# Kernel tuning notes

Hardware: AMD Instinct MI355X
Metric: run time of the kernel (lower is better)

## Reference

```python
import jax, jax.numpy as jnp
import numpy as np

# Module constants (from init_kwargs / defaults)
CIN, COUT = 128, 64
H, W = 256, 256
X0, X1 = -50.0, 50.0
Y0, Y1 = -50.0, 50.0
Z0, Z1 = -3.0, 5.0
XRES = (X1 - X0) / W
YRES = (Y1 - Y0) / H
EPS = 1e-5


def setup_inputs() -> dict:
    key = jax.random.key(0)
    ks = jax.random.split(key, 24)
    B, N = 4, 100000
    # Points: x,y in [-55,55], z in [-3.5,5.5] so some points fall outside range (tests valid mask)
    xy = jax.random.uniform(ks[0], (B, N, 2), minval=-55.0, maxval=55.0)
    z = jax.random.uniform(ks[1], (B, N, 1), minval=-3.5, maxval=5.5)
    points = jnp.concatenate([xy, z], axis=-1).astype(jnp.float32)
    features = jax.random.normal(ks[2], (B, N, CIN), dtype=jnp.float32)

    def lin(k, fan_in, shape):
        return jax.random.uniform(k, shape, minval=-1.0, maxval=1.0) / np.sqrt(fan_in)

    inp = dict(points=points, features=features)
    # point_mlp: Linear(131,64) -> BN1d(64) -> ReLU -> Linear(64,64)
    inp['w1'] = lin(ks[3], CIN + 3, (CIN + 3, COUT)).astype(jnp.float32)
    inp['b1'] = lin(ks[4], CIN + 3, (COUT,)).astype(jnp.float32)
    inp['bn1_g'] = jax.random.uniform(ks[5], (COUT,), minval=0.5, maxval=1.5)
    inp['bn1_b'] = 0.1 * jax.random.normal(ks[6], (COUT,))
    inp['bn1_m'] = 0.1 * jax.random.normal(ks[7], (COUT,))
    inp['bn1_v'] = jax.random.uniform(ks[8], (COUT,), minval=0.5, maxval=1.5)
    inp['w2'] = lin(ks[9], COUT, (COUT, COUT)).astype(jnp.float32)
    inp['b2'] = lin(ks[10], COUT, (COUT,)).astype(jnp.float32)
    # bev_conv: Conv(64,64,3)+BN2d+ReLU, Conv(64,64,3)+BN2d+ReLU  (OIHW kernels)
    fan = COUT * 9
    inp['cw1'] = lin(ks[11], fan, (COUT, COUT, 3, 3)).astype(jnp.float32)
    inp['cb1'] = lin(ks[12], fan, (COUT,)).astype(jnp.float32)
    inp['cbn1_g'] = jax.random.uniform(ks[13], (COUT,), minval=0.5, maxval=1.5)
    inp['cbn1_b'] = 0.1 * jax.random.normal(ks[14], (COUT,))
    inp['cbn1_m'] = 0.1 * jax.random.normal(ks[15], (COUT,))
    inp['cbn1_v'] = jax.random.uniform(ks[16], (COUT,), minval=0.5, maxval=1.5)
    inp['cw2'] = lin(ks[17], fan, (COUT, COUT, 3, 3)).astype(jnp.float32)
    inp['cb2'] = lin(ks[18], fan, (COUT,)).astype(jnp.float32)
    inp['cbn2_g'] = jax.random.uniform(ks[19], (COUT,), minval=0.5, maxval=1.5)
    inp['cbn2_b'] = 0.1 * jax.random.normal(ks[20], (COUT,))
    inp['cbn2_m'] = 0.1 * jax.random.normal(ks[21], (COUT,))
    inp['cbn2_v'] = jax.random.uniform(ks[22], (COUT,), minval=0.5, maxval=1.5)
    return {k: jnp.asarray(v, jnp.float32) for k, v in inp.items()}


def _bn(x, g, b, m, v, axis):
    shape = [1] * x.ndim
    shape[axis] = -1
    r = lambda a: a.reshape(shape)
    return (x - r(m)) * jax.lax.rsqrt(r(v) + EPS) * r(g) + r(b)


def _conv(x, w, b):
    y = jax.lax.conv_general_dilated(x, w, (1, 1), 'SAME',
                                     dimension_numbers=('NCHW', 'OIHW', 'NCHW'))
    return y + b[None, :, None, None]


def _forward(points, features, w1, b1, bn1_g, bn1_b, bn1_m, bn1_v, w2, b2,
             cw1, cb1, cbn1_g, cbn1_b, cbn1_m, cbn1_v,
             cw2, cb2, cbn2_g, cbn2_b, cbn2_m, cbn2_v):
    B, N, _ = features.shape
    x, y, z = points[..., 0], points[..., 1], points[..., 2]
    valid = ((x >= X0) & (x < X1) & (y >= Y0) & (y < Y1) & (z >= Z0) & (z < Z1))  # (B,N)
    col = jnp.clip(((x - X0) / XRES).astype(jnp.int32), 0, W - 1)
    row = jnp.clip(((y - Y0) / YRES).astype(jnp.int32), 0, H - 1)

    # position encoding (normalized coords)
    pos = jnp.stack([(x - X0) / (X1 - X0), (y - Y0) / (Y1 - Y0), (z - Z0) / (Z1 - Z0)], axis=-1)
    combined = jnp.concatenate([features, pos], axis=-1)  # (B,N,C+3)

    # point MLP (BN in inference mode with running stats)
    h = jnp.einsum('bnc,co->bno', combined, w1) + b1
    h = jax.nn.relu(_bn(h, bn1_g, bn1_b, bn1_m, bn1_v, axis=2))
    h = jnp.einsum('bnc,co->bno', h, w2) + b2  # (B,N,COUT)

    # scatter-max into BEV grid; bev initialized to zeros, so floor at 0
    seg = (jnp.arange(B, dtype=jnp.int32)[:, None] * H + row) * W + col  # (B,N)
    NEG = jnp.float32(-jnp.inf)
    vals = jnp.where(valid[..., None], h, NEG).reshape(B * N, COUT)
    m = jax.ops.segment_max(vals, seg.reshape(-1), num_segments=B * H * W)
    bev = jnp.maximum(m, 0.0).reshape(B, H, W, COUT).transpose(0, 3, 1, 2)  # (B,COUT,H,W)

    # BEV conv stack
    bev = jax.nn.relu(_bn(_conv(bev, cw1, cb1), cbn1_g, cbn1_b, cbn1_m, cbn1_v, axis=1))
    bev = jax.nn.relu(_bn(_conv(bev, cw2, cb2), cbn2_g, cbn2_b, cbn2_m, cbn2_v, axis=1))
    return bev


def reference(points, features, w1, b1, bn1_g, bn1_b, bn1_m, bn1_v, w2, b2,
              cw1, cb1, cbn1_g, cbn1_b, cbn1_m, cbn1_v,
              cw2, cb2, cbn2_g, cbn2_b, cbn2_m, cbn2_v):
    return _forward(points, features, w1, b1, bn1_g, bn1_b, bn1_m, bn1_v, w2, b2,
                    cw1, cb1, cbn1_g, cbn1_b, cbn1_m, cbn1_v,
                    cw2, cb2, cbn2_g, cbn2_b, cbn2_m, cbn2_v)
```

## Files before the change

kernel.cpp:

```cpp
#include <hip/hip_runtime.h>
#include <hip/hip_bf16.h>

typedef __attribute__((ext_vector_type(8))) short short8;
typedef __attribute__((ext_vector_type(4))) float floatx4;

static __device__ __forceinline__ unsigned short f2bf(float f) {
    unsigned int u = __float_as_uint(f);
    unsigned int r = (u + 0x7FFFu + ((u >> 16) & 1u)) >> 16;
    return (unsigned short)r;
}

static __device__ __forceinline__ short8 cvt8(const float* __restrict__ p) {
    const float4 f0 = *reinterpret_cast<const float4*>(p);
    const float4 f1 = *reinterpret_cast<const float4*>(p + 4);
    union { short8 s; __hip_bfloat162 h[4]; } u;
    u.h[0] = __float22bfloat162_rn(make_float2(f0.x, f0.y));
    u.h[1] = __float22bfloat162_rn(make_float2(f0.z, f0.w));
    u.h[2] = __float22bfloat162_rn(make_float2(f1.x, f1.y));
    u.h[3] = __float22bfloat162_rn(make_float2(f1.z, f1.w));
    return u.s;
}
static __device__ __forceinline__ uint4 cvt8u(const float* __restrict__ p) {
    const float4 f0 = *reinterpret_cast<const float4*>(p);
    const float4 f1 = *reinterpret_cast<const float4*>(p + 4);
    union { uint4 u; __hip_bfloat162 h[4]; } w;
    w.h[0] = __float22bfloat162_rn(make_float2(f0.x, f0.y));
    w.h[1] = __float22bfloat162_rn(make_float2(f0.z, f0.w));
    w.h[2] = __float22bfloat162_rn(make_float2(f1.x, f1.y));
    w.h[3] = __float22bfloat162_rn(make_float2(f1.z, f1.w));
    return w.u;
}

#define BATCH 4
#define NPTS 100000
#define CIN 128
#define COUT 64
#define HH 256
#define WW 256
#define HP 258
#define WP 258

#define OFF_BUF2 0
#define SZ_BUF   (BATCH * HP * WP * COUT * 2)
#define OFF_WB1  (OFF_BUF2 + SZ_BUF)
#define SZ_WB    (9 * COUT * COUT * 2)
#define OFF_WB2  (OFF_WB1 + SZ_WB)
#define OFF_BIAS1 (OFF_WB2 + SZ_WB)
#define OFF_BIAS2 (OFF_BIAS1 + 256)
#define OFF_W1T  (OFF_BIAS2 + 256)
#define OFF_W1POS (OFF_W1T + 64 * 128 * 2)
#define OFF_B1F  (OFF_W1POS + 768)
#define OFF_W2T  (OFF_B1F + 256)
#define OFF_B2F  (OFF_W2T + 64 * 64 * 2)

__global__ void prep_weights(const float* __restrict__ cw1, const float* __restrict__ cb1,
                             const float* __restrict__ g1, const float* __restrict__ bb1,
                             const float* __restrict__ m1, const float* __restrict__ v1,
                             const float* __restrict__ cw2, const float* __restrict__ cb2,
                             const float* __restrict__ g2, const float* __restrict__ bb2,
                             const float* __restrict__ m2, const float* __restrict__ v2,
                             unsigned short* __restrict__ Wb1, unsigned short* __restrict__ Wb2,
                             float* __restrict__ bias1, float* __restrict__ bias2) {
    int idx = blockIdx.x * 256 + threadIdx.x;
    int l = idx / 36864;
    int r = idx - l * 36864;
    int ci = r & 63;
    int co = (r >> 6) & 63;
    int tap = r >> 12;
    const float* w  = l ? cw2 : cw1;
    const float* g  = l ? g2  : g1;
    const float* v  = l ? v2  : v1;
    float s = g[co] * rsqrtf(v[co] + 1e-5f);
    float wv = w[(co * 64 + ci) * 9 + tap] * s;
    (l ? Wb2 : Wb1)[(tap * 64 + co) * 64 + ci] = f2bf(wv);
    if (tap == 0 && ci == 0) {
        const float* cb = l ? cb2 : cb1;
        const float* bb = l ? bb2 : bb1;
        const float* m  = l ? m2  : m1;
        (l ? bias2 : bias1)[co] = s * (cb[co] - m[co]) + bb[co];
    }
}

__global__ void prep_mlp(const float* __restrict__ w1, const float* __restrict__ b1,
                         const float* __restrict__ g, const float* __restrict__ bb,
                         const float* __restrict__ m, const float* __restrict__ v,
                         const float* __restrict__ w2, const float* __restrict__ b2,
                         unsigned short* __restrict__ w1T, float* __restrict__ w1pos,
                         float* __restrict__ b1f,
                         unsigned short* __restrict__ w2T, float* __restrict__ b2f) {
    int idx = blockIdx.x * 256 + threadIdx.x;
    if (idx < 8192) {
        int co = idx >> 7, k = idx & 127;
        float rs = g[co] * rsqrtf(v[co] + 1e-5f);
        w1T[idx] = f2bf(w1[k * 64 + co] * rs);
        if (k < 3) w1pos[k * 64 + co] = w1[(128 + k) * 64 + co] * rs;
        if (k == 0) b1f[co] = (b1[co] - m[co]) * rs + bb[co];
    }
    if (idx < 4096) {
        int co = idx >> 6, k = idx & 63;
        w2T[idx] = f2bf(w2[k * 64 + co]);
        if (k == 0) b2f[co] = b2[co];
    }
}

__global__ void ring_zero(unsigned short* __restrict__ buf2) {
    int idx = blockIdx.x * 256 + threadIdx.x;
    if (idx >= 4 * 1028 * 8) return;
    int c8 = idx & 7;
    int rest = idx >> 3;
    int p = rest % 1028;
    int b = rest / 1028;
    int x, y;
    if (p < 258)      { y = 0;   x = p; }
    else if (p < 516) { y = 257; x = p - 258; }
    else if (p < 772) { x = 0;   y = p - 516 + 1; }
    else              { x = 257; y = p - 772 + 1; }
    unsigned short* dst = buf2 + (((b * HP + y) * WP + x) * 64 + c8 * 8);
    uint4 z = {0u, 0u, 0u, 0u};
    *reinterpret_cast<uint4*>(dst) = z;
}

#define HSTR 72
#define VSTR 68
__global__ __launch_bounds__(256) void mlp_gemm_scatter(
        const float* __restrict__ points, const float* __restrict__ features,
        const unsigned short* __restrict__ w1T, const float* __restrict__ w1pos,
        const float* __restrict__ b1f,
        const unsigned short* __restrict__ w2T, const float* __restrict__ b2f,
        float* __restrict__ bev ) {
    __shared__ unsigned short ldsH[128 * HSTR];
    __shared__ unsigned short ldsV[128 * VSTR];
    __shared__ float4 ldsPos[128];

    const int tid = threadIdx.x;
    const int w = tid >> 6, lane = tid & 63, n = lane & 15, q = lane >> 4;
    const int m0 = w * 32;
    const long pt0 = (long)blockIdx.x * 128;

    if (lane < 32) {
        const long pt = pt0 + m0 + lane;
        const float x = points[pt * 3 + 0];
        const float y = points[pt * 3 + 1];
        const float z = points[pt * 3 + 2];
        const bool valid = (x >= -50.f) & (x < 50.f) & (y >= -50.f) & (y < 50.f) &
                           (z >= -3.f) & (z < 5.f);
        int cell = -1;
        if (valid) {
            int col = (int)((x + 50.f) / 0.390625f); col = min(max(col, 0), 255);
            int row = (int)((y + 50.f) / 0.390625f); row = min(max(row, 0), 255);
            int b = pt >= 300000 ? 3 : (pt >= 200000 ? 2 : (pt >= 100000 ? 1 : 0));
            cell = (b * HH + row) * WW + col;
        }
        float4 v;
        v.x = (x + 50.f) * 0.01f;
        v.y = (y + 50.f) * 0.01f;
        v.z = (z + 3.f) * 0.125f;
        v.w = __int_as_float(cell);
        ldsPos[m0 + lane] = v;
    }

    floatx4 acc[2][4];
    #pragma unroll
    for (int mt = 0; mt < 2; ++mt)
        #pragma unroll
        for (int nt = 0; nt < 4; ++nt) acc[mt][nt] = (floatx4){0.f, 0.f, 0.f, 0.f};

    #pragma unroll
    for (int ks = 0; ks < 4; ++ks) {
        short8 bf[4];
        #pragma unroll
        for (int nt = 0; nt < 4; ++nt)
            bf[nt] = *reinterpret_cast<const short8*>(w1T + (nt * 16 + n) * 128 + ks * 32 + q * 8);
        #pragma unroll
        for (int mt = 0; mt < 2; ++mt) {
            short8 a = cvt8(features + (pt0 + m0 + mt * 16 + n) * CIN + ks * 32 + q * 8);
            #pragma unroll
            for (int nt = 0; nt < 4; ++nt)
                acc[mt][nt] = __builtin_amdgcn_mfma_f32_16x16x32_bf16(a, bf[nt], acc[mt][nt], 0, 0, 0);
        }
    }

    float w1p[3][4], bs1[4];
    #pragma unroll
    for (int nt = 0; nt < 4; ++nt) {
        bs1[nt] = b1f[nt * 16 + n];
        #pragma unroll
        for (int j = 0; j < 3; ++j) w1p[j][nt] = w1pos[j * 64 + nt * 16 + n];
    }

    #pragma unroll
    for (int mt = 0; mt < 2; ++mt)
        #pragma unroll
        for (int r = 0; r < 4; ++r) {
            const int mm = m0 + mt * 16 + q * 4 + r;
            const float4 pos = ldsPos[mm];
            #pragma unroll
            for (int nt = 0; nt < 4; ++nt) {
                float hv = acc[mt][nt][r] + bs1[nt]
                         + pos.x * w1p[0][nt] + pos.y * w1p[1][nt] + pos.z * w1p[2][nt];
                ldsH[mm * HSTR + nt * 16 + n] = f2bf(fmaxf(hv, 0.f));
            }
        }

    floatx4 acc2[2][4];
    #pragma unroll
    for (int mt = 0; mt < 2; ++mt)
        #pragma unroll
        for (int nt = 0; nt < 4; ++nt) acc2[mt][nt] = (floatx4){0.f, 0.f, 0.f, 0.f};

    #pragma unroll
    for (int ks = 0; ks < 2; ++ks) {
        short8 bf[4];
        #pragma unroll
        for (int nt = 0; nt < 4; ++nt)
            bf[nt] = *reinterpret_cast<const short8*>(w2T + (nt * 16 + n) * 64 + ks * 32 + q * 8);
        #pragma unroll
        for (int mt = 0; mt < 2; ++mt) {
            short8 a = *reinterpret_cast<const short8*>(
                &ldsH[(m0 + mt * 16 + n) * HSTR + ks * 32 + q * 8]);
            #pragma unroll
            for (int nt = 0; nt < 4; ++nt)
                acc2[mt][nt] = __builtin_amdgcn_mfma_f32_16x16x32_bf16(a, bf[nt], acc2[mt][nt], 0, 0, 0);
        }
    }

    float bs2[4];
    #pragma unroll
    for (int nt = 0; nt < 4; ++nt) bs2[nt] = b2f[nt * 16 + n];

    #pragma unroll
    for (int mt = 0; mt < 2; ++mt)
        #pragma unroll
        for (int r = 0; r < 4; ++r) {
            const int mm = m0 + mt * 16 + q * 4 + r;
            #pragma unroll
            for (int nt = 0; nt < 4; ++nt) {
                float val = fmaxf(acc2[mt][nt][r] + bs2[nt], 0.f);
                ldsV[mm * VSTR + nt * 16 + n] = f2bf(val);
            }
        }

    #pragma unroll 4
    for (int i = 0; i < 32; ++i) {
        const int p = m0 + i;
        const int cell = __builtin_amdgcn_readfirstlane(__float_as_int(ldsPos[p].w));
        if (cell >= 0) {
            unsigned int bits = (unsigned int)ldsV[p * VSTR + lane] << 16;
            atomicMax((int*)bev + (long)cell * 64 + lane, (int)bits);
        }
    }
}

#define PSTR 72
template <bool FINAL, bool SRCF32>
__global__ __launch_bounds__(256) void conv3x3(const void* __restrict__ Xsrc,
                                               const unsigned short* __restrict__ Wb,
                                               const float* __restrict__ bias,
                                               void* __restrict__ out) {
    __shared__ unsigned short lds[3 * 66 * PSTR];

    const int bx = blockIdx.x;
    const int by = blockIdx.y;
    const int bz = blockIdx.z;
    const int tid = threadIdx.x;
    const int x0 = bx * 64;

    for (int ch = tid; ch < 1584; ch += 256) {
        int flat = ch * 8;
        int r = flat / 4224;
        int rem = flat - r * 4224;
        int p = rem >> 6;
        int ci = rem & 63;
        uint4 v;
        if (SRCF32) {
            int gy = by + r - 1;
            int gx = x0 + p - 1;
            if (gy >= 0 && gy < HH && gx >= 0 && gx < WW) {
                v = cvt8u((const float*)Xsrc + (((bz * HH + gy) * WW) + gx) * 64 + ci);
            } else {
                v = (uint4){0u, 0u, 0u, 0u};
            }
        } else {
            v = *reinterpret_cast<const uint4*>(
                (const unsigned short*)Xsrc + (((bz * HP + by + r) * WP) + x0 + p) * 64 + ci);
        }
        *reinterpret_cast<uint4*>(&lds[(r * 66 + p) * PSTR + ci]) = v;
    }

    const int wv = tid >> 6;
    const int lane = tid & 63;
    const int n = lane & 15;
    const int q = lane >> 4;

    short8 bfrag[9][2];
    #pragma unroll
    for (int t = 0; t < 9; ++t)
        #pragma unroll
        for (int kk = 0; kk < 2; ++kk)
            bfrag[t][kk] = *reinterpret_cast<const short8*>(
                Wb + ((t * 64 + wv * 16 + n) * 64 + kk * 32 + q * 8));

    __syncthreads();

    floatx4 acc[4];
    #pragma unroll
    for (int mt = 0; mt < 4; ++mt) acc[mt] = (floatx4){0.f, 0.f, 0.f, 0.f};

    #pragma unroll
    for (int t = 0; t < 9; ++t) {
        const int dy = t / 3, dx = t % 3;
        const int rowbase = dy * 66 * PSTR;
        #pragma unroll
        for (int kk = 0; kk < 2; ++kk) {
            const int cio = kk * 32 + q * 8;
            #pragma unroll
            for (int mt = 0; mt < 4; ++mt) {
                const int p = mt * 16 + n + dx;
                short8 a = *reinterpret_cast<const short8*>(&lds[rowbase + p * PSTR + cio]);
                acc[mt] = __builtin_amdgcn_mfma_f32_16x16x32_bf16(a, bfrag[t][kk], acc[mt], 0, 0, 0);
            }
        }
    }

    const int co = wv * 16 + n;
    const float bs = bias[co];
    #pragma unroll
    for (int mt = 0; mt < 4; ++mt) {
        #pragma unroll
        for (int r = 0; r < 4; ++r) {
            int px = mt * 16 + q * 4 + r;
            float val = fmaxf(acc[mt][r] + bs, 0.f);
            if (FINAL) {
                ((float*)out)[((bz * 64 + co) * HH + by) * WW + x0 + px] = val;
            } else {
                ((unsigned short*)out)[((bz * HP + by + 1) * WP + (x0 + px + 1)) * 64 + co] = f2bf(val);
            }
        }
    }
}

extern "C" void kernel_launch(void* const* d_in, const int* in_sizes, int n_in,
                              void* d_out, int out_size, void* d_ws, size_t ws_size,
                              hipStream_t stream) {
    const float* points   = (const float*)d_in[0];
    const float* features = (const float*)d_in[1];
    const float* w1   = (const float*)d_in[2];
    const float* b1   = (const float*)d_in[3];
    const float* bn1g = (const float*)d_in[4];
    const float* bn1b = (const float*)d_in[5];
    const float* bn1m = (const float*)d_in[6];
    const float* bn1v = (const float*)d_in[7];
    const float* w2   = (const float*)d_in[8];
    const float* b2   = (const float*)d_in[9];
    const float* cw1  = (const float*)d_in[10];
    const float* cb1  = (const float*)d_in[11];
    const float* cg1  = (const float*)d_in[12];
    const float* cbb1 = (const float*)d_in[13];
    const float* cm1  = (const float*)d_in[14];
    const float* cv1  = (const float*)d_in[15];
    const float* cw2  = (const float*)d_in[16];
    const float* cb2  = (const float*)d_in[17];
    const float* cg2  = (const float*)d_in[18];
    const float* cbb2 = (const float*)d_in[19];
    const float* cm2  = (const float*)d_in[20];
    const float* cv2  = (const float*)d_in[21];

    float* out = (float*)d_out;
    char* ws = (char*)d_ws;
    unsigned short* buf2 = (unsigned short*)(ws + OFF_BUF2);
    unsigned short* Wb1  = (unsigned short*)(ws + OFF_WB1);
    unsigned short* Wb2  = (unsigned short*)(ws + OFF_WB2);
    float* bias1 = (float*)(ws + OFF_BIAS1);
    float* bias2 = (float*)(ws + OFF_BIAS2);
    unsigned short* w1T = (unsigned short*)(ws + OFF_W1T);
    float* w1pos = (float*)(ws + OFF_W1POS);
    float* b1f = (float*)(ws + OFF_B1F);
    unsigned short* w2T = (unsigned short*)(ws + OFF_W2T);
    float* b2f = (float*)(ws + OFF_B2F);

    hipMemsetAsync(d_out, 0, (size_t)BATCH * HH * WW * COUT * 4, stream);
    ring_zero<<<(4 * 1028 * 8 + 255) / 256, 256, 0, stream>>>(buf2);

    prep_weights<<<288, 256, 0, stream>>>(cw1, cb1, cg1, cbb1, cm1, cv1,
                                          cw2, cb2, cg2, cbb2, cm2, cv2,
                                          Wb1, Wb2, bias1, bias2);
    prep_mlp<<<32, 256, 0, stream>>>(w1, b1, bn1g, bn1b, bn1m, bn1v, w2, b2,
                                     w1T, w1pos, b1f, w2T, b2f);

    mlp_gemm_scatter<<<(BATCH * NPTS) / 128, 256, 0, stream>>>(
        points, features, w1T, w1pos, b1f, w2T, b2f, out);

    dim3 cgrid(WW / 64, HH, BATCH);
    conv3x3<false, true><<<cgrid, 256, 0, stream>>>((const void*)out, Wb1, bias1, (void*)buf2);
    conv3x3<true, false><<<cgrid, 256, 0, stream>>>((const void*)buf2, Wb2, bias2, (void*)out);
}
```

Before: 490.7 us.

## Split MLP scatter into separate kernel and compute two rows per conv block

The MLP kernel now writes bf16 per-point outputs and cell indices to workspace, and a separate scatter_max kernel performs the atomic max into the BEV grid. This decouples the atomic-heavy phase from the MFMA GEMM so each can schedule independently. The conv kernels now compute two output rows per 512-thread block, loading four input rows into LDS instead of three per row, which cuts halo reload traffic. The cost is an extra round trip of about 51 MB through global memory, one more kernel launch, and more LDS per conv block.

```diff
diff --git a/kernel.cpp b/kernel.cpp
--- a/kernel.cpp
+++ b/kernel.cpp
@@ -33,6 +33,7 @@
 
 #define BATCH 4
 #define NPTS 100000
+#define NTOT (BATCH * NPTS)
 #define CIN 128
 #define COUT 64
 #define HH 256
@@ -52,6 +53,9 @@
 #define OFF_B1F  (OFF_W1POS + 768)
 #define OFF_W2T  (OFF_B1F + 256)
 #define OFF_B2F  (OFF_W2T + 64 * 64 * 2)
+#define OFF_PTS  (OFF_B2F + 256)
+#define SZ_PTS   (NTOT * COUT * 2)
+#define OFF_CELLS (OFF_PTS + SZ_PTS)
 
 __global__ void prep_weights(const float* __restrict__ cw1, const float* __restrict__ cb1,
                              const float* __restrict__ g1, const float* __restrict__ bb1,
@@ -121,13 +125,13 @@
 }
 
 #define HSTR 72
-#define VSTR 68
-__global__ __launch_bounds__(256) void mlp_gemm_scatter(
+#define VSTR 72
+__global__ __launch_bounds__(256) void mlp_gemm(
         const float* __restrict__ points, const float* __restrict__ features,
         const unsigned short* __restrict__ w1T, const float* __restrict__ w1pos,
         const float* __restrict__ b1f,
         const unsigned short* __restrict__ w2T, const float* __restrict__ b2f,
-        float* __restrict__ bev ) {
+        unsigned short* __restrict__ ptsOut, int* __restrict__ cellBuf) {
     __shared__ unsigned short ldsH[128 * HSTR];
     __shared__ unsigned short ldsV[128 * VSTR];
     __shared__ float4 ldsPos[128];
@@ -151,11 +155,12 @@
             int b = pt >= 300000 ? 3 : (pt >= 200000 ? 2 : (pt >= 100000 ? 1 : 0));
             cell = (b * HH + row) * WW + col;
         }
+        cellBuf[pt] = cell;
         float4 v;
         v.x = (x + 50.f) * 0.01f;
         v.y = (y + 50.f) * 0.01f;
         v.z = (z + 3.f) * 0.125f;
-        v.w = __int_as_float(cell);
+        v.w = 0.f;
         ldsPos[m0 + lane] = v;
     }
 
@@ -240,24 +245,41 @@
             }
         }
 
-    #pragma unroll 4
-    for (int i = 0; i < 32; ++i) {
-        const int p = m0 + i;
-        const int cell = __builtin_amdgcn_readfirstlane(__float_as_int(ldsPos[p].w));
-        if (cell >= 0) {
-            unsigned int bits = (unsigned int)ldsV[p * VSTR + lane] << 16;
-            atomicMax((int*)bev + (long)cell * 64 + lane, (int)bits);
+    #pragma unroll
+    for (int i4 = 0; i4 < 4; ++i4) {
+        const int pl = m0 + i4 * 8 + (lane >> 3);
+        const int ch = (lane & 7) * 8;
+        uint4 v = *reinterpret_cast<const uint4*>(&ldsV[pl * VSTR + ch]);
+        *reinterpret_cast<uint4*>(ptsOut + (pt0 + pl) * 64 + ch) = v;
+    }
+}
+
+__global__ __launch_bounds__(256) void scatter_max(
+        const unsigned short* __restrict__ ptsOut,
+        const int* __restrict__ cellBuf,
+        float* __restrict__ bev) {
+    const int w = threadIdx.x >> 6, lane = threadIdx.x & 63;
+    const long base = (long)blockIdx.x * 256 + w * 64;
+    int cell = -1;
+    if (base + lane < NTOT) cell = cellBuf[base + lane];
+    #pragma unroll
+    for (int i = 0; i < 64; ++i) {
+        const int c = __shfl(cell, i, 64);
+        if (c >= 0) {
+            unsigned int bits = (unsigned int)ptsOut[(base + i) * 64 + lane] << 16;
+            atomicMax((int*)bev + (long)c * 64 + lane, (int)bits);
         }
     }
 }
 
 #define PSTR 72
+#define CROWS 2
 template <bool FINAL, bool SRCF32>
-__global__ __launch_bounds__(256) void conv3x3(const void* __restrict__ Xsrc,
+__global__ __launch_bounds__(512) void conv3x3(const void* __restrict__ Xsrc,
                                                const unsigned short* __restrict__ Wb,
                                                const float* __restrict__ bias,
                                                void* __restrict__ out) {
-    __shared__ unsigned short lds[3 * 66 * PSTR];
+    __shared__ unsigned short lds[(CROWS + 2) * 66 * PSTR];
 
     const int bx = blockIdx.x;
     const int by = blockIdx.y;
@@ -265,7 +287,7 @@
     const int tid = threadIdx.x;
     const int x0 = bx * 64;
 
-    for (int ch = tid; ch < 1584; ch += 256) {
+    for (int ch = tid; ch < (CROWS + 2) * 66 * 8; ch += 512) {
         int flat = ch * 8;
         int r = flat / 4224;
         int rem = flat - r * 4224;
@@ -273,7 +295,7 @@
         int ci = rem & 63;
         uint4 v;
         if (SRCF32) {
-            int gy = by + r - 1;
+            int gy = by * CROWS + r - 1;
             int gx = x0 + p - 1;
             if (gy >= 0 && gy < HH && gx >= 0 && gx < WW) {
                 v = cvt8u((const float*)Xsrc + (((bz * HH + gy) * WW) + gx) * 64 + ci);
@@ -282,12 +304,14 @@
             }
         } else {
             v = *reinterpret_cast<const uint4*>(
-                (const unsigned short*)Xsrc + (((bz * HP + by + r) * WP) + x0 + p) * 64 + ci);
+                (const unsigned short*)Xsrc + (((bz * HP + by * CROWS + r) * WP) + x0 + p) * 64 + ci);
         }
         *reinterpret_cast<uint4*>(&lds[(r * 66 + p) * PSTR + ci]) = v;
     }
 
-    const int wv = tid >> 6;
+    const int w8 = tid >> 6;
+    const int rr = w8 >> 2;
+    const int wv = w8 & 3;
     const int lane = tid & 63;
     const int n = lane & 15;
     const int q = lane >> 4;
@@ -309,7 +333,7 @@
     #pragma unroll
     for (int t = 0; t < 9; ++t) {
         const int dy = t / 3, dx = t % 3;
-        const int rowbase = dy * 66 * PSTR;
+        const int rowbase = (rr + dy) * 66 * PSTR;
         #pragma unroll
         for (int kk = 0; kk < 2; ++kk) {
             const int cio = kk * 32 + q * 8;
@@ -323,6 +347,7 @@
     }
 
     const int co = wv * 16 + n;
+    const int yy = by * CROWS + rr;
     const float bs = bias[co];
     #pragma unroll
     for (int mt = 0; mt < 4; ++mt) {
@@ -331,9 +356,9 @@
             int px = mt * 16 + q * 4 + r;
             float val = fmaxf(acc[mt][r] + bs, 0.f);
             if (FINAL) {
-                ((float*)out)[((bz * 64 + co) * HH + by) * WW + x0 + px] = val;
+                ((float*)out)[((bz * 64 + co) * HH + yy) * WW + x0 + px] = val;
             } else {
-                ((unsigned short*)out)[((bz * HP + by + 1) * WP + (x0 + px + 1)) * 64 + co] = f2bf(val);
+                ((unsigned short*)out)[((bz * HP + yy + 1) * WP + (x0 + px + 1)) * 64 + co] = f2bf(val);
             }
         }
     }
@@ -377,6 +402,8 @@
     float* b1f = (float*)(ws + OFF_B1F);
     unsigned short* w2T = (unsigned short*)(ws + OFF_W2T);
     float* b2f = (float*)(ws + OFF_B2F);
+    unsigned short* ptsOut = (unsigned short*)(ws + OFF_PTS);
+    int* cellBuf = (int*)(ws + OFF_CELLS);
 
     hipMemsetAsync(d_out, 0, (size_t)BATCH * HH * WW * COUT * 4, stream);
     ring_zero<<<(4 * 1028 * 8 + 255) / 256, 256, 0, stream>>>(buf2);
@@ -387,10 +414,12 @@
     prep_mlp<<<32, 256, 0, stream>>>(w1, b1, bn1g, bn1b, bn1m, bn1v, w2, b2,
                                      w1T, w1pos, b1f, w2T, b2f);
 
-    mlp_gemm_scatter<<<(BATCH * NPTS) / 128, 256, 0, stream>>>(
-        points, features, w1T, w1pos, b1f, w2T, b2f, out);
-
-    dim3 cgrid(WW / 64, HH, BATCH);
-    conv3x3<false, true><<<cgrid, 256, 0, stream>>>((const void*)out, Wb1, bias1, (void*)buf2);
-    conv3x3<true, false><<<cgrid, 256, 0, stream>>>((const void*)buf2, Wb2, bias2, (void*)out);
-}
+    mlp_gemm<<<NTOT / 128, 256, 0, stream>>>(
+        points, features, w1T, w1pos, b1f, w2T, b2f, ptsOut, cellBuf);
+
+    scatter_max<<<(NTOT + 255) / 256, 256, 0, stream>>>(ptsOut, cellBuf, out);
+
+    dim3 cgrid(WW / 64, HH / CROWS, BATCH);
+    conv3x3<false, true><<<cgrid, 512, 0, stream>>>((const void*)out, Wb1, bias1, (void*)buf2);
+    conv3x3<true, false><<<cgrid, 512, 0, stream>>>((const void*)buf2, Wb2, bias2, (void*)out);
+}
```

Measured after the change: 532.3 us. +8.5%, slower.

## Tile conv3x3 over four output rows per block with per-wave full channel tiles

Applied to the files above, without the earlier changes.

Each conv block now computes four output rows instead of one, loading a 6-row halo into LDS rather than 3 rows per output row. This cuts redundant halo loads by about half. Each wave now owns one output row and computes all 64 output channels, so a single A fragment feeds four MFMAs. Weights are loaded per tap inside the loop instead of being preloaded. Accumulator registers rise to 64 floats per lane and LDS doubles, which can lower occupancy and adds weight reloads from global/L1.

```diff
diff --git a/kernel.cpp b/kernel.cpp
--- a/kernel.cpp
+++ b/kernel.cpp
@@ -33,6 +33,7 @@
 
 #define BATCH 4
 #define NPTS 100000
+#define NTOT (BATCH * NPTS)
 #define CIN 128
 #define COUT 64
 #define HH 256
@@ -257,23 +258,23 @@
                                                const unsigned short* __restrict__ Wb,
                                                const float* __restrict__ bias,
                                                void* __restrict__ out) {
-    __shared__ unsigned short lds[3 * 66 * PSTR];
+    __shared__ unsigned short lds[6 * 66 * PSTR];
 
     const int bx = blockIdx.x;
     const int by = blockIdx.y;
     const int bz = blockIdx.z;
     const int tid = threadIdx.x;
     const int x0 = bx * 64;
-
-    for (int ch = tid; ch < 1584; ch += 256) {
-        int flat = ch * 8;
-        int r = flat / 4224;
-        int rem = flat - r * 4224;
-        int p = rem >> 6;
-        int ci = rem & 63;
+    const int y0 = by * 4;
+
+    for (int ch = tid; ch < 3168; ch += 256) {
+        int r = ch / 528;
+        int rem = ch - r * 528;
+        int p = rem >> 3;
+        int ci = (rem & 7) * 8;
         uint4 v;
         if (SRCF32) {
-            int gy = by + r - 1;
+            int gy = y0 + r - 1;
             int gx = x0 + p - 1;
             if (gy >= 0 && gy < HH && gx >= 0 && gx < WW) {
                 v = cvt8u((const float*)Xsrc + (((bz * HH + gy) * WW) + gx) * 64 + ci);
@@ -282,58 +283,68 @@
             }
         } else {
             v = *reinterpret_cast<const uint4*>(
-                (const unsigned short*)Xsrc + (((bz * HP + by + r) * WP) + x0 + p) * 64 + ci);
+                (const unsigned short*)Xsrc + (((bz * HP + y0 + r) * WP) + x0 + p) * 64 + ci);
         }
         *reinterpret_cast<uint4*>(&lds[(r * 66 + p) * PSTR + ci]) = v;
     }
 
-    const int wv = tid >> 6;
+    const int w = tid >> 6;
     const int lane = tid & 63;
     const int n = lane & 15;
     const int q = lane >> 4;
 
-    short8 bfrag[9][2];
-    #pragma unroll
-    for (int t = 0; t < 9; ++t)
-        #pragma unroll
-        for (int kk = 0; kk < 2; ++kk)
-            bfrag[t][kk] = *reinterpret_cast<const short8*>(
-                Wb + ((t * 64 + wv * 16 + n) * 64 + kk * 32 + q * 8));
-
     __syncthreads();
 
-    floatx4 acc[4];
-    #pragma unroll
-    for (int mt = 0; mt < 4; ++mt) acc[mt] = (floatx4){0.f, 0.f, 0.f, 0.f};
+    floatx4 acc[4][4];
+    #pragma unroll
+    for (int mt = 0; mt < 4; ++mt)
+        #pragma unroll
+        for (int nt = 0; nt < 4; ++nt) acc[mt][nt] = (floatx4){0.f, 0.f, 0.f, 0.f};
 
     #pragma unroll
     for (int t = 0; t < 9; ++t) {
         const int dy = t / 3, dx = t % 3;
-        const int rowbase = dy * 66 * PSTR;
+        short8 bf[2][4];
+        #pragma unroll
+        for (int kk = 0; kk < 2; ++kk)
+            #pragma unroll
+            for (int nt = 0; nt < 4; ++nt)
+                bf[kk][nt] = *reinterpret_cast<const short8*>(
+                    Wb + ((t * 64 + nt * 16 + n) * 64 + kk * 32 + q * 8));
+        const int rowbase = (w + dy) * 66 * PSTR;
         #pragma unroll
         for (int kk = 0; kk < 2; ++kk) {
             const int cio = kk * 32 + q * 8;
-            #pragma unroll
-            for (int mt = 0; mt < 4; ++mt) {
-                const int p = mt * 16 + n + dx;
-                short8 a = *reinterpret_cast<const short8*>(&lds[rowbase + p * PSTR + cio]);
-                acc[mt] = __builtin_amdgcn_mfma_f32_16x16x32_bf16(a, bfrag[t][kk], acc[mt], 0, 0, 0);
-            }
-        }
-    }
-
-    const int co = wv * 16 + n;
-    const float bs = bias[co];
-    #pragma unroll
-    for (int mt = 0; mt < 4; ++mt) {
-        #pragma unroll
-        for (int r = 0; r < 4; ++r) {
-            int px = mt * 16 + q * 4 + r;
-            float val = fmaxf(acc[mt][r] + bs, 0.f);
-            if (FINAL) {
-                ((float*)out)[((bz * 64 + co) * HH + by) * WW + x0 + px] = val;
-            } else {
-                ((unsigned short*)out)[((bz * HP + by + 1) * WP + (x0 + px + 1)) * 64 + co] = f2bf(val);
+            short8 a[4];
+            #pragma unroll
+            for (int mt = 0; mt < 4; ++mt)
+                a[mt] = *reinterpret_cast<const short8*>(
+                    &lds[rowbase + (mt * 16 + n + dx) * PSTR + cio]);
+            #pragma unroll
+            for (int mt = 0; mt < 4; ++mt)
+                #pragma unroll
+                for (int nt = 0; nt < 4; ++nt)
+                    acc[mt][nt] = __builtin_amdgcn_mfma_f32_16x16x32_bf16(
+                        a[mt], bf[kk][nt], acc[mt][nt], 0, 0, 0);
+        }
+    }
+
+    const int yy = y0 + w;
+    #pragma unroll
+    for (int nt = 0; nt < 4; ++nt) {
+        const int co = nt * 16 + n;
+        const float bs = bias[co];
+        #pragma unroll
+        for (int mt = 0; mt < 4; ++mt) {
+            #pragma unroll
+            for (int r = 0; r < 4; ++r) {
+                int px = mt * 16 + q * 4 + r;
+                float val = fmaxf(acc[mt][nt][r] + bs, 0.f);
+                if (FINAL) {
+                    ((float*)out)[((bz * 64 + co) * HH + yy) * WW + x0 + px] = val;
+                } else {
+                    ((unsigned short*)out)[((bz * HP + yy + 1) * WP + (x0 + px + 1)) * 64 + co] = f2bf(val);
+                }
             }
         }
     }
@@ -387,10 +398,10 @@
     prep_mlp<<<32, 256, 0, stream>>>(w1, b1, bn1g, bn1b, bn1m, bn1v, w2, b2,
                                      w1T, w1pos, b1f, w2T, b2f);
 
-    mlp_gemm_scatter<<<(BATCH * NPTS) / 128, 256, 0, stream>>>(
+    mlp_gemm_scatter<<<NTOT / 128, 256, 0, stream>>>(
         points, features, w1T, w1pos, b1f, w2T, b2f, out);
 
-    dim3 cgrid(WW / 64, HH, BATCH);
+    dim3 cgrid(WW / 64, HH / 4, BATCH);
     conv3x3<false, true><<<cgrid, 256, 0, stream>>>((const void*)out, Wb1, bias1, (void*)buf2);
     conv3x3<true, false><<<cgrid, 256, 0, stream>>>((const void*)buf2, Wb2, bias2, (void*)out);
 }
```

After: 502.0 us. 1.02x slower.
